# Performance work log

Hardware: AMD Instinct MI355X
Metric: run time of the kernel (lower is better)

The kernel has to match this reference:

```python
import jax, jax.numpy as jnp
import numpy as np
from jax import lax

TOP_K = 2
ROUTED_SCALING = 1.0
Q_MAX = 127.0


def setup_inputs() -> dict:
    key = jax.random.key(0)
    ks = jax.random.split(key, 7)
    B, S, H, I, E = 4, 2048, 2048, 1408, 8
    hidden_states = jax.random.normal(ks[0], (B, S, H), dtype=jnp.float32)
    gate_w = jax.random.normal(ks[1], (E, H), dtype=jnp.float32) * 0.02
    w13_q = jax.random.randint(ks[2], (E, 2 * I, H), -127, 128, dtype=jnp.int32)
    w13_scale = jax.random.uniform(ks[3], (E, 2 * I), dtype=jnp.float32, minval=0.5, maxval=1.5) * 0.01
    w2_q = jax.random.randint(ks[4], (E, H, I), -127, 128, dtype=jnp.int32)
    w2_scale = jax.random.uniform(ks[5], (E, H), dtype=jnp.float32, minval=0.5, maxval=1.5) * 0.01
    shared_output = jax.random.normal(ks[6], (B * S, H), dtype=jnp.float32)
    return {
        "hidden_states": hidden_states,
        "gate_w": gate_w,
        "w13_q": w13_q,
        "w13_scale": w13_scale,
        "w2_q": w2_q,
        "w2_scale": w2_scale,
        "shared_output": shared_output,
    }


def _dyn_quant_i8(x):
    """Per-token symmetric dynamic int8 quantization. Returns (q, scale)."""
    s = jnp.max(jnp.abs(x), axis=-1, keepdims=True) / Q_MAX
    s = jnp.maximum(s, 1e-8)
    q = jnp.clip(jnp.round(x / s), -Q_MAX, Q_MAX)
    return q, s


def reference(hidden_states, gate_w, w13_q, w13_scale, w2_q, w2_scale, shared_output):
    B, S, H = hidden_states.shape
    E = w13_q.shape[0]
    I = w2_q.shape[2]
    x = hidden_states.reshape(B * S, H)  # [T, H]

    # --- gating: fp32 linear + top-k softmax (renormalize=True) ---
    logits = jnp.einsum("th,eh->te", x, gate_w)
    probs = jax.nn.softmax(logits, axis=-1)
    gates, topk_idx = lax.top_k(probs, TOP_K)  # [T, K]
    gates = gates / jnp.sum(gates, axis=-1, keepdims=True)

    # --- dynamic per-token int8 quantization of activations ---
    xq, xs = _dyn_quant_i8(x)  # [T, H], [T, 1]

    # --- grouped int8 GEMM MoE, scanned over experts (faithful to
    # token-sorted grouped GEMM: each token is processed by each of its
    # top-k experts; here we compute per expert and mask/weight-combine). ---
    def body(acc, packed):
        w13_e, s13_e, w2_e, s2_e, e = packed
        # fc1 (w8a8, TN): dequant via per-token input scale * per-row weight scale
        h = (xq @ w13_e.astype(jnp.float32).T) * xs * s13_e[None, :]  # [T, 2I]
        # fused SwiGLU + dynamic int8 re-quant
        a = jax.nn.silu(h[:, :I]) * h[:, I:]
        aq, a_s = _dyn_quant_i8(a)
        # fc2 (w8a8, TN)
        y = (aq @ w2_e.astype(jnp.float32).T) * a_s * s2_e[None, :]  # [T, H]
        # gate weight for tokens routed to this expert (0 otherwise)
        w_tok = jnp.sum(jnp.where(topk_idx == e, gates, 0.0), axis=-1)  # [T]
        return acc + w_tok[:, None] * y, None

    acc0 = jnp.zeros((B * S, H), jnp.float32)
    acc, _ = lax.scan(body, acc0, (w13_q, w13_scale, w2_q, w2_scale, jnp.arange(E)))

    # --- combine: routed scaling + shared-expert residual ---
    return ROUTED_SCALING * acc + shared_output
```

## Files before the change

### kernel.cpp

```cpp
#include <hip/hip_runtime.h>
#include <hip/hip_bf16.h>
#include <math.h>

#define TOKS 8192
#define HD   2048
#define ID   1408
#define NE   8
#define N13  2816

typedef int v4i __attribute__((ext_vector_type(4)));

__device__ __forceinline__ void async_copy16(const signed char* g, signed char* l) {
    __builtin_amdgcn_global_load_lds(
        (const __attribute__((address_space(1))) void*)g,
        (__attribute__((address_space(3))) void*)l, 16, 0, 0);
}

__global__ __launch_bounds__(256) void gate_quant_kernel(
    const float* __restrict__ x, const float* __restrict__ gw,
    signed char* __restrict__ xq, float* __restrict__ xs,
    float* __restrict__ gates, unsigned char* __restrict__ ex_of_slot)
{
    const int t = blockIdx.x;
    const int tid = threadIdx.x;
    const float* xr = x + (size_t)t * HD + tid * 8;
    const float4 xa = *(const float4*)(xr);
    const float4 xb = *(const float4*)(xr + 4);
    float acc[NE];
#pragma unroll
    for (int e = 0; e < NE; ++e) {
        const float* wr = gw + e * HD + tid * 8;
        float4 wa = *(const float4*)(wr);
        float4 wb = *(const float4*)(wr + 4);
        acc[e] = xa.x*wa.x + xa.y*wa.y + xa.z*wa.z + xa.w*wa.w +
                 xb.x*wb.x + xb.y*wb.y + xb.z*wb.z + xb.w*wb.w;
    }
    float am = fmaxf(fmaxf(fmaxf(fabsf(xa.x), fabsf(xa.y)), fmaxf(fabsf(xa.z), fabsf(xa.w))),
                     fmaxf(fmaxf(fabsf(xb.x), fabsf(xb.y)), fmaxf(fabsf(xb.z), fabsf(xb.w))));
#pragma unroll
    for (int off = 1; off < 64; off <<= 1) {
#pragma unroll
        for (int e = 0; e < NE; ++e) acc[e] += __shfl_xor(acc[e], off);
        am = fmaxf(am, __shfl_xor(am, off));
    }
    __shared__ float red[4][9];
    __shared__ float logit_s[8];
    __shared__ float sbc;
    const int wv = tid >> 6;
    if ((tid & 63) == 0) {
#pragma unroll
        for (int e = 0; e < NE; ++e) red[wv][e] = acc[e];
        red[wv][8] = am;
    }
    __syncthreads();
    if (tid < 8) logit_s[tid] = red[0][tid] + red[1][tid] + red[2][tid] + red[3][tid];
    if (tid == 8) {
        const float amx = fmaxf(fmaxf(red[0][8], red[1][8]), fmaxf(red[2][8], red[3][8]));
        const float s = fmaxf(amx / 127.0f, 1e-8f);
        xs[t] = s;
        sbc = s;
    }
    __syncthreads();
    if (tid == 0) {
        float l[NE];
#pragma unroll
        for (int e = 0; e < NE; ++e) l[e] = logit_s[e];
        int e0 = 0;
#pragma unroll
        for (int e = 1; e < NE; ++e) if (l[e] > l[e0]) e0 = e;
        int e1 = (e0 == 0) ? 1 : 0;
#pragma unroll
        for (int e = 0; e < NE; ++e) if (e != e0 && l[e] > l[e1]) e1 = e;
        const float d = expf(l[e1] - l[e0]);
        gates[2*t]     = 1.0f / (1.0f + d);
        gates[2*t + 1] = d / (1.0f + d);
        uchar2 p; p.x = (unsigned char)e0; p.y = (unsigned char)e1;
        *(uchar2*)(ex_of_slot + 2 * t) = p;
    }
    const float s = sbc;
    const float v[8] = {xa.x, xa.y, xa.z, xa.w, xb.x, xb.y, xb.z, xb.w};
    unsigned int lo = 0, hi = 0;
#pragma unroll
    for (int i = 0; i < 4; ++i) {
        int q = (int)fminf(fmaxf(rintf(v[i] / s), -127.f), 127.f);
        lo |= ((unsigned)(q & 0xff)) << (8 * i);
    }
#pragma unroll
    for (int i = 0; i < 4; ++i) {
        int q = (int)fminf(fmaxf(rintf(v[4 + i] / s), -127.f), 127.f);
        hi |= ((unsigned)(q & 0xff)) << (8 * i);
    }
    int2 pk; pk.x = (int)lo; pk.y = (int)hi;
    *(int2*)(xq + (size_t)t * HD + tid * 8) = pk;
}

__global__ __launch_bounds__(256) void build_lists_kernel(
    const unsigned char* __restrict__ ex_of_slot,
    int* __restrict__ counts, int* __restrict__ lists)
{
    const int e = blockIdx.x;
    const int tid = threadIdx.x;
    const int lane = tid & 63;
    const int wv = tid >> 6;
    __shared__ int wsum[4];
    __shared__ int base;
    if (tid == 0) base = 0;
    __syncthreads();
    int* mylist = lists + e * TOKS;
    for (int it = 0; it < 2 * TOKS / 256; ++it) {
        const int slot = it * 256 + tid;
        const bool m = (ex_of_slot[slot] == (unsigned char)e);
        const unsigned long long mask = __ballot(m);
        const int wprefix = __popcll(mask & ((1ULL << lane) - 1ULL));
        if (lane == 0) wsum[wv] = __popcll(mask);
        __syncthreads();
        int wbase = base;
        for (int w = 0; w < wv; ++w) wbase += wsum[w];
        if (m) mylist[wbase + wprefix] = slot;
        __syncthreads();
        if (tid == 0) base += wsum[0] + wsum[1] + wsum[2] + wsum[3];
        __syncthreads();
    }
    if (tid == 0) counts[e] = base;
}

__global__ __launch_bounds__(256) void convert_w13_kernel(
    const int* __restrict__ wq, signed char* __restrict__ w8)
{
    const unsigned idx = blockIdx.x * 256u + threadIdx.x;
    const unsigned kq = idx & 511u;
    const unsigned rowq = idx >> 9;
    const unsigned np = rowq % 2816u;
    const unsigned e = rowq / 2816u;
    const unsigned inrow = ((np >> 4) & 1u) * 1408u + (np >> 5) * 16u + (np & 15u);
    const int4 vv = *(const int4*)(wq + (size_t)(e * 2816u + inrow) * 2048u + kq * 4u);
    char4 c;
    c.x = (signed char)vv.x; c.y = (signed char)vv.y;
    c.z = (signed char)vv.z; c.w = (signed char)vv.w;
    *(char4*)(w8 + (size_t)rowq * 2048u + kq * 4u) = c;
}

__global__ __launch_bounds__(256) void convert_w2_kernel(
    const int* __restrict__ wq, signed char* __restrict__ w8)
{
    const size_t idx = (size_t)blockIdx.x * 256 + threadIdx.x;
    const int4 vv = *(const int4*)(wq + idx * 4);
    char4 c;
    c.x = (signed char)vv.x; c.y = (signed char)vv.y;
    c.z = (signed char)vv.z; c.w = (signed char)vv.w;
    *(char4*)(w8 + idx * 4) = c;
}

__global__ __launch_bounds__(256) void copy_out_kernel(
    const float* __restrict__ src, float* __restrict__ dst)
{
    const size_t idx = (size_t)blockIdx.x * 256 + threadIdx.x;
    ((float4*)dst)[idx] = ((const float4*)src)[idx];
}

__global__ __launch_bounds__(256, 2) void fc1_kernel(
    const signed char* __restrict__ xq, const signed char* __restrict__ w13_8,
    const float* __restrict__ xs, const float* __restrict__ w13s,
    const int* __restrict__ counts, const int* __restrict__ lists,
    __hip_bfloat16* __restrict__ a_buf, unsigned int* __restrict__ amax)
{
    const int e = blockIdx.z;
    const int n_e = counts[e];
    const int m0 = blockIdx.y * 128;
    if (m0 >= n_e) return;
    const int n0 = blockIdx.x * 128;
    const int* list = lists + e * TOKS;
    const signed char* B = w13_8 + (size_t)e * N13 * HD;

    __shared__ signed char lsA[128 * 64];
    __shared__ signed char lsB[128 * 64];

    const int tid = threadIdx.x;
    const int wv = tid >> 6;
    const int l  = tid & 63;
    const int r4 = l >> 2;
    const int c4 = l & 3;
    const int k16 = c4 ^ (r4 & 3);

    const int rowA0 = m0 + wv * 32 + r4;
    const int rowA1 = rowA0 + 16;
    const int slotA0 = (rowA0 < n_e) ? list[rowA0] : 0;
    const int slotA1 = (rowA1 < n_e) ? list[rowA1] : 0;
    const signed char* gA0 = xq + (size_t)(slotA0 >> 1) * HD + k16 * 16;
    const signed char* gA1 = xq + (size_t)(slotA1 >> 1) * HD + k16 * 16;
    const signed char* gB0 = B + (size_t)(n0 + wv * 32 + r4) * HD + k16 * 16;
    const signed char* gB1 = gB0 + (size_t)16 * HD;
    signed char* ldsA0 = lsA + (wv * 2 + 0) * 1024;
    signed char* ldsA1 = lsA + (wv * 2 + 1) * 1024;
    signed char* ldsB0 = lsB + (wv * 2 + 0) * 1024;
    signed char* ldsB1 = lsB + (wv * 2 + 1) * 1024;

    const int quad = l >> 4, jj = l & 15;
    const int wm = (wv >> 1) * 64, wn = (wv & 1) * 64;
    const int swz = ((quad ^ (jj & 3)) * 16);

    const v4i zero = {0, 0, 0, 0};
    v4i acc[4][4];
#pragma unroll
    for (int a = 0; a < 4; ++a)
#pragma unroll
        for (int b = 0; b < 4; ++b) acc[a][b] = zero;

    for (int kc = 0; kc < 32; ++kc) {
        const int k0 = kc * 64;
        __syncthreads();
        async_copy16(gA0 + k0, ldsA0);
        async_copy16(gA1 + k0, ldsA1);
        async_copy16(gB0 + k0, ldsB0);
        async_copy16(gB1 + k0, ldsB1);
        __syncthreads();
        v4i af[4], bf[4];
#pragma unroll
        for (int mi = 0; mi < 4; ++mi)
            af[mi] = *(const v4i*)(lsA + (wm + mi * 16 + jj) * 64 + swz);
#pragma unroll
        for (int ni = 0; ni < 4; ++ni)
            bf[ni] = *(const v4i*)(lsB + (wn + ni * 16 + jj) * 64 + swz);
#pragma unroll
        for (int mi = 0; mi < 4; ++mi)
#pragma unroll
            for (int ni = 0; ni < 4; ++ni)
                acc[mi][ni] = __builtin_amdgcn_mfma_i32_16x16x64_i8(af[mi], bf[ni], acc[mi][ni], 0, 0, 0);
    }

    const float* s13e = w13s + e * N13;
    const int qbase = (n0 + wn) >> 5;
#pragma unroll
    for (int mi = 0; mi < 4; ++mi) {
#pragma unroll
        for (int r = 0; r < 4; ++r) {
            const int idx = m0 + wm + mi * 16 + quad * 4 + r;
            const bool valid = (idx < n_e);
            int slot = 0; float xsv = 0.f;
            if (valid) { slot = list[idx]; xsv = xs[slot >> 1]; }
            float rowmax = 0.f;
            float avals[2];
#pragma unroll
            for (int p = 0; p < 2; ++p) {
                const int q = qbase + p;
                const float sg = s13e[q * 16 + jj];
                const float su = s13e[ID + q * 16 + jj];
                const float hg = (float)acc[mi][2 * p][r] * xsv * sg;
                const float hu = (float)acc[mi][2 * p + 1][r] * xsv * su;
                const float av = hg / (1.0f + expf(-hg)) * hu;
                avals[p] = av;
                rowmax = fmaxf(rowmax, fabsf(av));
            }
            rowmax = fmaxf(rowmax, __shfl_xor(rowmax, 1));
            rowmax = fmaxf(rowmax, __shfl_xor(rowmax, 2));
            rowmax = fmaxf(rowmax, __shfl_xor(rowmax, 4));
            rowmax = fmaxf(rowmax, __shfl_xor(rowmax, 8));
            if (valid) {
                __hip_bfloat16* arow = a_buf + (size_t)slot * ID;
#pragma unroll
                for (int p = 0; p < 2; ++p)
                    arow[(qbase + p) * 16 + jj] = __float2bfloat16(avals[p]);
                if (jj == 0) atomicMax(amax + slot, __float_as_uint(rowmax));
            }
        }
    }
}

__global__ __launch_bounds__(192) void requant_kernel(
    const __hip_bfloat16* __restrict__ a_buf, const unsigned int* __restrict__ amax,
    float* __restrict__ a_s, signed char* __restrict__ aq)
{
    const int row = blockIdx.x;
    const float am = __uint_as_float(amax[row]);
    const float s = fmaxf(am / 127.0f, 1e-8f);
    if (threadIdx.x == 0) a_s[row] = s;
    const unsigned short* ar = (const unsigned short*)(a_buf + (size_t)row * ID);
    signed char* qr = aq + (size_t)row * ID;
    const float inv = 1.0f / s;
    for (int c = threadIdx.x; c < ID / 8; c += 192) {
        union { int4 v; unsigned short u[8]; } dat;
        dat.v = *(const int4*)(ar + c * 8);
        unsigned int lo = 0, hi = 0;
#pragma unroll
        for (int i = 0; i < 4; ++i) {
            const float f = __uint_as_float((unsigned)dat.u[i] << 16);
            int q = (int)fminf(fmaxf(rintf(f * inv), -127.f), 127.f);
            lo |= ((unsigned)(q & 0xff)) << (8 * i);
        }
#pragma unroll
        for (int i = 0; i < 4; ++i) {
            const float f = __uint_as_float((unsigned)dat.u[4 + i] << 16);
            int q = (int)fminf(fmaxf(rintf(f * inv), -127.f), 127.f);
            hi |= ((unsigned)(q & 0xff)) << (8 * i);
        }
        int2 pk; pk.x = (int)lo; pk.y = (int)hi;
        *(int2*)(qr + c * 8) = pk;
    }
}

__global__ __launch_bounds__(256, 2) void fc2_kernel(
    const signed char* __restrict__ aq, const signed char* __restrict__ w2_8,
    const float* __restrict__ a_s, const float* __restrict__ w2s,
    const float* __restrict__ gates,
    const int* __restrict__ counts, const int* __restrict__ lists,
    float* __restrict__ out)
{
    const int e = blockIdx.z;
    const int n_e = counts[e];
    const int m0 = blockIdx.y * 128;
    if (m0 >= n_e) return;
    const int n0 = blockIdx.x * 128;
    const int* list = lists + e * TOKS;
    const signed char* B = w2_8 + (size_t)e * HD * ID;

    __shared__ signed char lsA[128 * 64];
    __shared__ signed char lsB[128 * 64];

    const int tid = threadIdx.x;
    const int wv = tid >> 6;
    const int l  = tid & 63;
    const int r4 = l >> 2;
    const int c4 = l & 3;
    const int k16 = c4 ^ (r4 & 3);

    const int rowA0 = m0 + wv * 32 + r4;
    const int rowA1 = rowA0 + 16;
    const int slotA0 = (rowA0 < n_e) ? list[rowA0] : 0;
    const int slotA1 = (rowA1 < n_e) ? list[rowA1] : 0;
    const signed char* gA0 = aq + (size_t)slotA0 * ID + k16 * 16;
    const signed char* gA1 = aq + (size_t)slotA1 * ID + k16 * 16;
    const signed char* gB0 = B + (size_t)(n0 + wv * 32 + r4) * ID + k16 * 16;
    const signed char* gB1 = gB0 + (size_t)16 * ID;
    signed char* ldsA0 = lsA + (wv * 2 + 0) * 1024;
    signed char* ldsA1 = lsA + (wv * 2 + 1) * 1024;
    signed char* ldsB0 = lsB + (wv * 2 + 0) * 1024;
    signed char* ldsB1 = lsB + (wv * 2 + 1) * 1024;

    const int quad = l >> 4, jj = l & 15;
    const int wm = (wv >> 1) * 64, wn = (wv & 1) * 64;
    const int swz = ((quad ^ (jj & 3)) * 16);

    const v4i zero = {0, 0, 0, 0};
    v4i acc[4][4];
#pragma unroll
    for (int a = 0; a < 4; ++a)
#pragma unroll
        for (int b = 0; b < 4; ++b) acc[a][b] = zero;

    for (int kc = 0; kc < 22; ++kc) {
        const int k0 = kc * 64;
        __syncthreads();
        async_copy16(gA0 + k0, ldsA0);
        async_copy16(gA1 + k0, ldsA1);
        async_copy16(gB0 + k0, ldsB0);
        async_copy16(gB1 + k0, ldsB1);
        __syncthreads();
        v4i af[4], bf[4];
#pragma unroll
        for (int mi = 0; mi < 4; ++mi)
            af[mi] = *(const v4i*)(lsA + (wm + mi * 16 + jj) * 64 + swz);
#pragma unroll
        for (int ni = 0; ni < 4; ++ni)
            bf[ni] = *(const v4i*)(lsB + (wn + ni * 16 + jj) * 64 + swz);
#pragma unroll
        for (int mi = 0; mi < 4; ++mi)
#pragma unroll
            for (int ni = 0; ni < 4; ++ni)
                acc[mi][ni] = __builtin_amdgcn_mfma_i32_16x16x64_i8(af[mi], bf[ni], acc[mi][ni], 0, 0, 0);
    }

    const float* s2e = w2s + e * HD;
    float s2v[4];
#pragma unroll
    for (int ni = 0; ni < 4; ++ni) s2v[ni] = s2e[n0 + wn + ni * 16 + jj];
#pragma unroll
    for (int mi = 0; mi < 4; ++mi) {
#pragma unroll
        for (int r = 0; r < 4; ++r) {
            const int idx = m0 + wm + mi * 16 + quad * 4 + r;
            if (idx >= n_e) continue;
            const int slot = list[idx];
            const float coef = a_s[slot] * gates[slot];
            float* orow = out + (size_t)(slot >> 1) * HD + n0 + wn;
#pragma unroll
            for (int ni = 0; ni < 4; ++ni)
                atomicAdd(orow + ni * 16 + jj, (float)acc[mi][ni][r] * coef * s2v[ni]);
        }
    }
}

extern "C" void kernel_launch(void* const* d_in, const int* in_sizes, int n_in,
                              void* d_out, int out_size, void* d_ws, size_t ws_size,
                              hipStream_t stream)
{
    const float* x      = (const float*)d_in[0];
    const float* gw     = (const float*)d_in[1];
    const int*   w13q   = (const int*)d_in[2];
    const float* w13s   = (const float*)d_in[3];
    const int*   w2q    = (const int*)d_in[4];
    const float* w2s    = (const float*)d_in[5];
    const float* shared = (const float*)d_in[6];
    float* out = (float*)d_out;
    char* ws = (char*)d_ws;

    constexpr size_t SZ_W13 = (size_t)NE * N13 * HD;
    constexpr size_t SZ_W2  = (size_t)NE * HD * ID;
    constexpr size_t SZ_XQ  = (size_t)TOKS * HD;
    constexpr size_t SZ_AQ  = (size_t)2 * TOKS * ID;
    constexpr size_t SZ_A   = SZ_AQ * 2;
    constexpr size_t OFF_W13 = 0;
    constexpr size_t OFF_W2  = OFF_W13 + SZ_W13;
    constexpr size_t OFF_XQ  = OFF_W2 + SZ_W2;
    constexpr size_t OFF_AQ  = OFF_XQ + SZ_XQ;
    constexpr size_t OFF_A   = OFF_AQ + SZ_AQ;
    constexpr size_t OFF_XS  = OFF_A + SZ_A;
    constexpr size_t OFF_AS  = OFF_XS + 65536;
    constexpr size_t OFF_G   = OFF_AS + 65536;
    constexpr size_t OFF_AM  = OFF_G + 65536;
    constexpr size_t OFF_EX  = OFF_AM + 65536;
    constexpr size_t OFF_CNT = OFF_EX + 16384;
    constexpr size_t OFF_LST = OFF_CNT + 256;

    signed char* w13_8 = (signed char*)(ws + OFF_W13);
    signed char* w2_8  = (signed char*)(ws + OFF_W2);
    signed char* xq    = (signed char*)(ws + OFF_XQ);
    signed char* aqb   = (signed char*)(ws + OFF_AQ);
    __hip_bfloat16* a_buf = (__hip_bfloat16*)(ws + OFF_A);
    float* xs    = (float*)(ws + OFF_XS);
    float* a_s   = (float*)(ws + OFF_AS);
    float* gates = (float*)(ws + OFF_G);
    unsigned int* amax = (unsigned int*)(ws + OFF_AM);
    unsigned char* ex_of_slot = (unsigned char*)(ws + OFF_EX);
    int* counts = (int*)(ws + OFF_CNT);
    int* lists  = (int*)(ws + OFF_LST);

    hipMemsetAsync(amax, 0, 65536, stream);

    gate_quant_kernel<<<TOKS, 256, 0, stream>>>(x, gw, xq, xs, gates, ex_of_slot);
    build_lists_kernel<<<NE, 256, 0, stream>>>(ex_of_slot, counts, lists);
    convert_w13_kernel<<<(NE * N13 * (HD / 4)) / 256, 256, 0, stream>>>(w13q, w13_8);
    convert_w2_kernel<<<(NE * HD * (ID / 4)) / 256, 256, 0, stream>>>(w2q, w2_8);
    copy_out_kernel<<<(TOKS * HD / 4) / 256, 256, 0, stream>>>(shared, out);
    fc1_kernel<<<dim3(N13 / 128, 64, NE), 256, 0, stream>>>(
        xq, w13_8, xs, w13s, counts, lists, a_buf, amax);
    requant_kernel<<<2 * TOKS, 192, 0, stream>>>(a_buf, amax, a_s, aqb);
    fc2_kernel<<<dim3(HD / 128, 64, NE), 256, 0, stream>>>(
        aqb, w2_8, a_s, w2s, gates, counts, lists, out);
}
```

Before: 818.9 us.

## Load GEMM fragments directly from global into registers with double buffering

Both grouped int8 GEMM kernels stop staging A/B tiles through LDS with async global-to-LDS copies and two barriers per K step. Each lane now loads its MFMA fragments straight from global memory into registers, with a two-stage register prefetch that overlaps the next K slice's loads with the current MFMAs. This removes the LDS traffic and the block-wide syncs. In exchange, operands shared across waves are no longer reused through LDS, so each wave refetches A and B from global/L2, and register pressure rises.

After: 1.173 ms. +43.3%, slower.

```diff
diff --git a/kernel.cpp b/kernel.cpp
--- a/kernel.cpp
+++ b/kernel.cpp
@@ -9,12 +9,6 @@
 #define N13  2816
 
 typedef int v4i __attribute__((ext_vector_type(4)));
-
-__device__ __forceinline__ void async_copy16(const signed char* g, signed char* l) {
-    __builtin_amdgcn_global_load_lds(
-        (const __attribute__((address_space(1))) void*)g,
-        (__attribute__((address_space(3))) void*)l, 16, 0, 0);
-}
 
 __global__ __launch_bounds__(256) void gate_quant_kernel(
     const float* __restrict__ x, const float* __restrict__ gw,
@@ -172,32 +166,23 @@
     const int* list = lists + e * TOKS;
     const signed char* B = w13_8 + (size_t)e * N13 * HD;
 
-    __shared__ signed char lsA[128 * 64];
-    __shared__ signed char lsB[128 * 64];
-
     const int tid = threadIdx.x;
     const int wv = tid >> 6;
     const int l  = tid & 63;
-    const int r4 = l >> 2;
-    const int c4 = l & 3;
-    const int k16 = c4 ^ (r4 & 3);
-
-    const int rowA0 = m0 + wv * 32 + r4;
-    const int rowA1 = rowA0 + 16;
-    const int slotA0 = (rowA0 < n_e) ? list[rowA0] : 0;
-    const int slotA1 = (rowA1 < n_e) ? list[rowA1] : 0;
-    const signed char* gA0 = xq + (size_t)(slotA0 >> 1) * HD + k16 * 16;
-    const signed char* gA1 = xq + (size_t)(slotA1 >> 1) * HD + k16 * 16;
-    const signed char* gB0 = B + (size_t)(n0 + wv * 32 + r4) * HD + k16 * 16;
-    const signed char* gB1 = gB0 + (size_t)16 * HD;
-    signed char* ldsA0 = lsA + (wv * 2 + 0) * 1024;
-    signed char* ldsA1 = lsA + (wv * 2 + 1) * 1024;
-    signed char* ldsB0 = lsB + (wv * 2 + 0) * 1024;
-    signed char* ldsB1 = lsB + (wv * 2 + 1) * 1024;
-
     const int quad = l >> 4, jj = l & 15;
     const int wm = (wv >> 1) * 64, wn = (wv & 1) * 64;
-    const int swz = ((quad ^ (jj & 3)) * 16);
+
+    const signed char* aP[4];
+    const signed char* bP[4];
+#pragma unroll
+    for (int mi = 0; mi < 4; ++mi) {
+        const int ridx = m0 + wm + mi * 16 + jj;
+        const int slot = (ridx < n_e) ? list[ridx] : 0;
+        aP[mi] = xq + (size_t)(slot >> 1) * HD + quad * 16;
+    }
+#pragma unroll
+    for (int ni = 0; ni < 4; ++ni)
+        bP[ni] = B + (size_t)(n0 + wn + ni * 16 + jj) * HD + quad * 16;
 
     const v4i zero = {0, 0, 0, 0};
     v4i acc[4][4];
@@ -206,26 +191,37 @@
 #pragma unroll
         for (int b = 0; b < 4; ++b) acc[a][b] = zero;
 
-    for (int kc = 0; kc < 32; ++kc) {
-        const int k0 = kc * 64;
-        __syncthreads();
-        async_copy16(gA0 + k0, ldsA0);
-        async_copy16(gA1 + k0, ldsA1);
-        async_copy16(gB0 + k0, ldsB0);
-        async_copy16(gB1 + k0, ldsB1);
-        __syncthreads();
-        v4i af[4], bf[4];
+    v4i a0[4], b0[4], a1[4], b1[4];
+#pragma unroll
+    for (int i = 0; i < 4; ++i) {
+        a0[i] = *(const v4i*)(aP[i]);
+        b0[i] = *(const v4i*)(bP[i]);
+    }
+    for (int kc = 0; kc < 32; kc += 2) {
+        const int k1 = (kc + 1) * 64;
+#pragma unroll
+        for (int i = 0; i < 4; ++i) {
+            a1[i] = *(const v4i*)(aP[i] + k1);
+            b1[i] = *(const v4i*)(bP[i] + k1);
+        }
 #pragma unroll
         for (int mi = 0; mi < 4; ++mi)
-            af[mi] = *(const v4i*)(lsA + (wm + mi * 16 + jj) * 64 + swz);
-#pragma unroll
-        for (int ni = 0; ni < 4; ++ni)
-            bf[ni] = *(const v4i*)(lsB + (wn + ni * 16 + jj) * 64 + swz);
+#pragma unroll
+            for (int ni = 0; ni < 4; ++ni)
+                acc[mi][ni] = __builtin_amdgcn_mfma_i32_16x16x64_i8(a0[mi], b0[ni], acc[mi][ni], 0, 0, 0);
+        if (kc + 2 < 32) {
+            const int k2 = (kc + 2) * 64;
+#pragma unroll
+            for (int i = 0; i < 4; ++i) {
+                a0[i] = *(const v4i*)(aP[i] + k2);
+                b0[i] = *(const v4i*)(bP[i] + k2);
+            }
+        }
 #pragma unroll
         for (int mi = 0; mi < 4; ++mi)
 #pragma unroll
             for (int ni = 0; ni < 4; ++ni)
-                acc[mi][ni] = __builtin_amdgcn_mfma_i32_16x16x64_i8(af[mi], bf[ni], acc[mi][ni], 0, 0, 0);
+                acc[mi][ni] = __builtin_amdgcn_mfma_i32_16x16x64_i8(a1[mi], b1[ni], acc[mi][ni], 0, 0, 0);
     }
 
     const float* s13e = w13s + e * N13;
@@ -313,32 +309,23 @@
     const int* list = lists + e * TOKS;
     const signed char* B = w2_8 + (size_t)e * HD * ID;
 
-    __shared__ signed char lsA[128 * 64];
-    __shared__ signed char lsB[128 * 64];
-
     const int tid = threadIdx.x;
     const int wv = tid >> 6;
     const int l  = tid & 63;
-    const int r4 = l >> 2;
-    const int c4 = l & 3;
-    const int k16 = c4 ^ (r4 & 3);
-
-    const int rowA0 = m0 + wv * 32 + r4;
-    const int rowA1 = rowA0 + 16;
-    const int slotA0 = (rowA0 < n_e) ? list[rowA0] : 0;
-    const int slotA1 = (rowA1 < n_e) ? list[rowA1] : 0;
-    const signed char* gA0 = aq + (size_t)slotA0 * ID + k16 * 16;
-    const signed char* gA1 = aq + (size_t)slotA1 * ID + k16 * 16;
-    const signed char* gB0 = B + (size_t)(n0 + wv * 32 + r4) * ID + k16 * 16;
-    const signed char* gB1 = gB0 + (size_t)16 * ID;
-    signed char* ldsA0 = lsA + (wv * 2 + 0) * 1024;
-    signed char* ldsA1 = lsA + (wv * 2 + 1) * 1024;
-    signed char* ldsB0 = lsB + (wv * 2 + 0) * 1024;
-    signed char* ldsB1 = lsB + (wv * 2 + 1) * 1024;
-
     const int quad = l >> 4, jj = l & 15;
     const int wm = (wv >> 1) * 64, wn = (wv & 1) * 64;
-    const int swz = ((quad ^ (jj & 3)) * 16);
+
+    const signed char* aP[4];
+    const signed char* bP[4];
+#pragma unroll
+    for (int mi = 0; mi < 4; ++mi) {
+        const int ridx = m0 + wm + mi * 16 + jj;
+        const int slot = (ridx < n_e) ? list[ridx] : 0;
+        aP[mi] = aq + (size_t)slot * ID + quad * 16;
+    }
+#pragma unroll
+    for (int ni = 0; ni < 4; ++ni)
+        bP[ni] = B + (size_t)(n0 + wn + ni * 16 + jj) * ID + quad * 16;
 
     const v4i zero = {0, 0, 0, 0};
     v4i acc[4][4];
@@ -347,26 +334,37 @@
 #pragma unroll
         for (int b = 0; b < 4; ++b) acc[a][b] = zero;
 
-    for (int kc = 0; kc < 22; ++kc) {
-        const int k0 = kc * 64;
-        __syncthreads();
-        async_copy16(gA0 + k0, ldsA0);
-        async_copy16(gA1 + k0, ldsA1);
-        async_copy16(gB0 + k0, ldsB0);
-        async_copy16(gB1 + k0, ldsB1);
-        __syncthreads();
-        v4i af[4], bf[4];
+    v4i a0[4], b0[4], a1[4], b1[4];
+#pragma unroll
+    for (int i = 0; i < 4; ++i) {
+        a0[i] = *(const v4i*)(aP[i]);
+        b0[i] = *(const v4i*)(bP[i]);
+    }
+    for (int kc = 0; kc < 22; kc += 2) {
+        const int k1 = (kc + 1) * 64;
+#pragma unroll
+        for (int i = 0; i < 4; ++i) {
+            a1[i] = *(const v4i*)(aP[i] + k1);
+            b1[i] = *(const v4i*)(bP[i] + k1);
+        }
 #pragma unroll
         for (int mi = 0; mi < 4; ++mi)
-            af[mi] = *(const v4i*)(lsA + (wm + mi * 16 + jj) * 64 + swz);
-#pragma unroll
-        for (int ni = 0; ni < 4; ++ni)
-            bf[ni] = *(const v4i*)(lsB + (wn + ni * 16 + jj) * 64 + swz);
+#pragma unroll
+            for (int ni = 0; ni < 4; ++ni)
+                acc[mi][ni] = __builtin_amdgcn_mfma_i32_16x16x64_i8(a0[mi], b0[ni], acc[mi][ni], 0, 0, 0);
+        if (kc + 2 < 22) {
+            const int k2 = (kc + 2) * 64;
+#pragma unroll
+            for (int i = 0; i < 4; ++i) {
+                a0[i] = *(const v4i*)(aP[i] + k2);
+                b0[i] = *(const v4i*)(bP[i] + k2);
+            }
+        }
 #pragma unroll
         for (int mi = 0; mi < 4; ++mi)
 #pragma unroll
             for (int ni = 0; ni < 4; ++ni)
-                acc[mi][ni] = __builtin_amdgcn_mfma_i32_16x16x64_i8(af[mi], bf[ni], acc[mi][ni], 0, 0, 0);
+                acc[mi][ni] = __builtin_amdgcn_mfma_i32_16x16x64_i8(a1[mi], b1[ni], acc[mi][ni], 0, 0, 0);
     }
 
     const float* s2e = w2s + e * HD;
```
